# Kernel optimization log

Measured on AMD Instinct MI355X. Metric: run time of the kernel, lower is better.

## Reference

```python
import jax, jax.numpy as jnp
import numpy as np

N = 50000      # nodes
E = 400000     # edges (before self-loops)
IN = 128       # in_channels
OUT = 64       # out_channels (per-head; concat=False averages heads)
HEADS = 8      # heads of first GAT layer; second layer has 1 head
NEG_SLOPE = 0.2


def _glorot(key, shape, fan_in, fan_out):
    s = jnp.sqrt(2.0 / (fan_in + fan_out)).astype(jnp.float32)
    return jax.random.normal(key, shape, jnp.float32) * s


def setup_inputs() -> dict:
    key = jax.random.key(0)
    ks = jax.random.split(key, 10)
    x = jax.random.normal(ks[0], (N, IN), jnp.float32)
    edge_index = jax.random.randint(ks[1], (2, E), 0, N)
    # layer 1: heads=HEADS, per-head dim OUT
    W1 = _glorot(ks[2], (IN, HEADS * OUT), IN, HEADS * OUT)
    att_src1 = _glorot(ks[3], (HEADS, OUT), OUT, 1)
    att_dst1 = _glorot(ks[4], (HEADS, OUT), OUT, 1)
    b1 = jnp.zeros((OUT,), jnp.float32)
    # layer 2: heads=1
    W2 = _glorot(ks[5], (OUT, 1 * OUT), OUT, OUT)
    att_src2 = _glorot(ks[6], (1, OUT), OUT, 1)
    att_dst2 = _glorot(ks[7], (1, OUT), OUT, 1)
    b2 = jnp.zeros((OUT,), jnp.float32)
    return dict(x=x, edge_index=edge_index, W1=W1, att_src1=att_src1,
                att_dst1=att_dst1, b1=b1, W2=W2, att_src2=att_src2,
                att_dst2=att_dst2, b2=b2)


def gat_conv(x, edge_index, W, att_src, att_dst, bias, heads, ch):
    """PyG GATConv with concat=False (mean over heads), add_self_loops=True."""
    n = x.shape[0]
    loop = jnp.arange(n, dtype=edge_index.dtype)
    src = jnp.concatenate([edge_index[0], loop])  # [E+N]
    dst = jnp.concatenate([edge_index[1], loop])
    h = (x @ W).reshape(n, heads, ch)                     # [N, H, C]
    a_s = jnp.sum(h * att_src, axis=-1)                   # [N, H]
    a_d = jnp.sum(h * att_dst, axis=-1)                   # [N, H]
    e = jax.nn.leaky_relu(a_s[src] + a_d[dst], NEG_SLOPE)  # [E+N, H]
    # numerically stable segment softmax over incoming edges of each dst node
    emax = jax.lax.stop_gradient(
        jax.ops.segment_max(e, dst, num_segments=n))       # [N, H]
    ee = jnp.exp(e - emax[dst])
    denom = jax.ops.segment_sum(ee, dst, num_segments=n)  # [N, H]
    alpha = ee / denom[dst]                                # [E+N, H]
    out = jax.ops.segment_sum(alpha[:, :, None] * h[src], dst,
                              num_segments=n)              # [N, H, C]
    return out.mean(axis=1) + bias                         # [N, C]


def reference(x, edge_index, W1, att_src1, att_dst1, b1,
              W2, att_src2, att_dst2, b2):
    h = gat_conv(x, edge_index, W1, att_src1, att_dst1, b1, HEADS, OUT)
    h = jax.nn.elu(h)
    return gat_conv(h, edge_index, W2, att_src2, att_dst2, b2, 1, OUT)
```

## Files before the change

kernel.cpp:

```cpp
#include <hip/hip_runtime.h>
#include <cstdint>
#include <cstddef>

#define NEG_SLOPE 0.2f

typedef short bf16x8 __attribute__((ext_vector_type(8)));
typedef float f32x4 __attribute__((ext_vector_type(4)));
typedef float f32x2 __attribute__((ext_vector_type(2)));

__device__ __forceinline__ unsigned short f2bf(float f) {
  unsigned u = __float_as_uint(f);
  u = u + 0x7FFFu + ((u >> 16) & 1u);
  return (unsigned short)(u >> 16);
}
__device__ __forceinline__ float bf2f(unsigned short b) {
  return __uint_as_float((unsigned)b << 16);
}
__device__ __forceinline__ f32x2 unpk(unsigned xv) {
  f32x2 r;
  r.x = __uint_as_float(xv << 16);
  r.y = __uint_as_float(xv & 0xFFFF0000u);
  return r;
}
__device__ __forceinline__ float rlf(float v, int l) {
  return __uint_as_float(
      (unsigned)__builtin_amdgcn_readlane((int)__float_as_uint(v), l));
}
__device__ __forceinline__ void dma16(const unsigned short* g, unsigned short* l) {
  __builtin_amdgcn_global_load_lds(
      (const __attribute__((address_space(1))) unsigned*)g,
      (__attribute__((address_space(3))) unsigned*)l, 16, 0, 0);
}

__global__ __launch_bounds__(256) void prep_all(
    const int* __restrict__ ei, int* __restrict__ counts,
    const float* __restrict__ x, unsigned short* __restrict__ xb,
    const float* __restrict__ W1, const float* __restrict__ att_s1,
    const float* __restrict__ att_d1, unsigned short* __restrict__ AsAdT,
    unsigned short* __restrict__ WbT,
    const float* __restrict__ W2, unsigned short* __restrict__ W2t,
    const float* __restrict__ att_s2, const float* __restrict__ att_d2,
    float* __restrict__ AsAd2,
    int E, int ET, int N, int B0, int B1) {
  int b = blockIdx.x, tid = threadIdx.x;
  if (b < B0) {
    int i = b * 256 + tid;
    if (i < ET) {
      int dst = (i < E) ? ei[E + i] : (i - E);
      atomicAdd(&counts[dst], 1);
    }
    return;
  }
  b -= B0;
  if (b < B1) {
    int i = b * 256 + tid;
    if (i < N * 32) {
      float4 v = ((const float4*)x)[i];
      ushort4 o;
      o.x = f2bf(v.x); o.y = f2bf(v.y); o.z = f2bf(v.z); o.w = f2bf(v.w);
      ((ushort4*)xb)[i] = o;
    }
    return;
  }
  b -= B1;
  if (b < 8) {
    int i = b * 256 + tid;
    int o = i >> 7, k = i & 127, h = o & 7;
    const float* att = (o < 8) ? att_s1 : att_d1;
    float s = 0.f;
    for (int c = 0; c < 64; c++) s += W1[(size_t)k * 512 + h * 64 + c] * att[h * 64 + c];
    AsAdT[i] = f2bf(s);
    return;
  }
  b -= 8;
  if (b < 256) {
    int i = b * 256 + tid;
    int o = i >> 10, k = i & 1023, h = k >> 7, c = k & 127;
    WbT[i] = f2bf(W1[(size_t)c * 512 + h * 64 + o]);
    return;
  }
  b -= 256;
  if (b < 16) {
    int i = b * 256 + tid;
    if (i < 64 * 64) {
      int k = i >> 6, nn = i & 63;
      W2t[(size_t)nn * 64 + k] = f2bf(W2[i]);
    }
    return;
  }
  {
    int i = tid;
    if (i < 128) {
      int o = i >> 6, k = i & 63;
      const float* att = (o == 0) ? att_s2 : att_d2;
      float s = 0.f;
      for (int c = 0; c < 64; c++) s += W2[(size_t)k * 64 + c] * att[c];
      AsAd2[i] = s;
    }
  }
}

__global__ __launch_bounds__(1024) void scan_dots(
    const int* __restrict__ counts, int* __restrict__ offsets,
    const unsigned short* __restrict__ xb, const unsigned short* __restrict__ AsAdT,
    float* __restrict__ asd, int n) {
  if (blockIdx.x == 0) {
    __shared__ int sums[1024];
    int t = threadIdx.x;
    int chunk = (n + 1023) >> 10;
    int start = t * chunk;
    int end = min(start + chunk, n);
    int s = 0;
    for (int i = start; i < end; i++) s += counts[i];
    sums[t] = s;
    __syncthreads();
    for (int off = 1; off < 1024; off <<= 1) {
      int v = (t >= off) ? sums[t - off] : 0;
      __syncthreads();
      sums[t] += v;
      __syncthreads();
    }
    int run = sums[t] - s;
    for (int i = start; i < end; i++) { offsets[i] = run; run += counts[i]; }
    if (t == 1023) offsets[n] = sums[1023];
    return;
  }
  int tid = threadIdx.x;
  int wave = tid >> 6, lane = tid & 63;
  int q = lane >> 4, t = lane & 15;
  int row0 = (blockIdx.x - 1) * 256 + wave * 16;
  int arow = row0 + t; if (arow > n - 1) arow = n - 1;
  const bf16x8* aptr = (const bf16x8*)(xb + (size_t)arow * 128);
  const bf16x8* bptr = (const bf16x8*)(AsAdT + t * 128);
  f32x4 acc = (f32x4){0.f, 0.f, 0.f, 0.f};
  #pragma unroll
  for (int s = 0; s < 4; s++)
    acc = __builtin_amdgcn_mfma_f32_16x16x32_bf16(aptr[s * 4 + q], bptr[s * 4 + q],
                                                  acc, 0, 0, 0);
  #pragma unroll
  for (int r = 0; r < 4; r++) {
    int row = row0 + q * 4 + r;
    if (row < n) asd[row * 16 + t] = acc[r];
  }
}

__global__ __launch_bounds__(256) void fill_csr(
    const int* __restrict__ ei, const int* __restrict__ offsets,
    int* __restrict__ cursor, int* __restrict__ srcs, int E, int ET) {
  int i = blockIdx.x * 256 + threadIdx.x;
  if (i >= ET) return;
  int src, dst;
  if (i < E) { src = ei[i]; dst = ei[E + i]; } else { src = dst = i - E; }
  int pos = atomicAdd(&cursor[dst], 1);
  srcs[offsets[dst] + pos] = src;
}

#define CONSUME8(STG, W, ACC)                                         \
  _Pragma("unroll")                                                   \
  for (int k = 0; k < 8; k++) {                                       \
    unsigned xv = *(const unsigned*)&(STG)[k * 128 + 2 * lane];       \
    f32x2 x2 = unpk(xv);                                              \
    ACC[0] += x2 * rlf(W, k * 8 + 0);                                 \
    ACC[1] += x2 * rlf(W, k * 8 + 1);                                 \
    ACC[2] += x2 * rlf(W, k * 8 + 2);                                 \
    ACC[3] += x2 * rlf(W, k * 8 + 3);                                 \
    ACC[4] += x2 * rlf(W, k * 8 + 4);                                 \
    ACC[5] += x2 * rlf(W, k * 8 + 5);                                 \
    ACC[6] += x2 * rlf(W, k * 8 + 6);                                 \
    ACC[7] += x2 * rlf(W, k * 8 + 7);                                 \
  }

__global__ __launch_bounds__(512, 4) void agg1_gemm(
    const int* __restrict__ offsets, const int* __restrict__ srcs,
    const float* __restrict__ asd, const unsigned short* __restrict__ xb,
    const unsigned short* __restrict__ WbT, const float* __restrict__ b1,
    const float* __restrict__ AsAd2, unsigned short* __restrict__ zb,
    float* __restrict__ as2, float* __restrict__ ad2, int N) {
  __shared__ unsigned short sh[16 * 2048];
  int tid = threadIdx.x;
  int wv = tid >> 6, lane = tid & 63;
  int nb = blockIdx.x;
  {
    int nodeA = nb * 16 + 2 * wv;
    unsigned short* stgA = &sh[(2 * wv) * 2048];
    unsigned short* stgB = &sh[(2 * wv + 1) * 2048];
    f32x2 accA[8], accB[8];
    #pragma unroll
    for (int h = 0; h < 8; h++) {
      accA[h] = (f32x2){0.f, 0.f};
      accB[h] = (f32x2){0.f, 0.f};
    }
    float wslA = 0.f, wslB = 0.f;
    int begA = offsets[nodeA];
    int endA = offsets[nodeA + 1];
    int endB = offsets[nodeA + 2];
    int begB = endA;
    int jlA = endA - 1, jlB = endB - 1;
    float advA = asd[(size_t)nodeA * 16 + 8 + (lane & 7)];
    float advB = asd[(size_t)(nodeA + 1) * 16 + 8 + (lane & 7)];
    for (int c = 0;; c += 16) {
      int cbA = begA + c, cbB = begB + c;
      bool hA = cbA < endA, hB = cbB < endB;
      if (!hA && !hB) break;
      int cntA = endA - cbA, cntB = endB - cbB;
      int sA0 = 0, sA1 = 0, sA2 = 0, sA3 = 0;
      int sB0 = 0, sB1 = 0, sB2 = 0, sB3 = 0;
      float asvaA = 0.f, asvbA = 0.f, asvaB = 0.f, asvbB = 0.f;
      if (hA) {
        sA0 = srcs[min(cbA + (lane >> 4), jlA)];
        sA1 = srcs[min(cbA + 4 + (lane >> 4), jlA)];
        int sw = srcs[min(cbA + (lane >> 3), jlA)];
        asvaA = asd[(size_t)sw * 16 + (lane & 7)];
        if (cntA > 8) {
          sA2 = srcs[min(cbA + 8 + (lane >> 4), jlA)];
          sA3 = srcs[min(cbA + 12 + (lane >> 4), jlA)];
          int sw2 = srcs[min(cbA + 8 + (lane >> 3), jlA)];
          asvbA = asd[(size_t)sw2 * 16 + (lane & 7)];
        }
      }
      if (hB) {
        sB0 = srcs[min(cbB + (lane >> 4), jlB)];
        sB1 = srcs[min(cbB + 4 + (lane >> 4), jlB)];
        int sw = srcs[min(cbB + (lane >> 3), jlB)];
        asvaB = asd[(size_t)sw * 16 + (lane & 7)];
        if (cntB > 8) {
          sB2 = srcs[min(cbB + 8 + (lane >> 4), jlB)];
          sB3 = srcs[min(cbB + 12 + (lane >> 4), jlB)];
          int sw2 = srcs[min(cbB + 8 + (lane >> 3), jlB)];
          asvbB = asd[(size_t)sw2 * 16 + (lane & 7)];
        }
      }
      if (hA) {
        dma16(xb + (size_t)(unsigned)sA0 * 128 + (lane & 15) * 8, stgA);
        dma16(xb + (size_t)(unsigned)sA1 * 128 + (lane & 15) * 8, stgA + 512);
        if (cntA > 8) {
          dma16(xb + (size_t)(unsigned)sA2 * 128 + (lane & 15) * 8, stgA + 1024);
          dma16(xb + (size_t)(unsigned)sA3 * 128 + (lane & 15) * 8, stgA + 1536);
        }
      }
      if (hB) {
        dma16(xb + (size_t)(unsigned)sB0 * 128 + (lane & 15) * 8, stgB);
        dma16(xb + (size_t)(unsigned)sB1 * 128 + (lane & 15) * 8, stgB + 512);
        if (cntB > 8) {
          dma16(xb + (size_t)(unsigned)sB2 * 128 + (lane & 15) * 8, stgB + 1024);
          dma16(xb + (size_t)(unsigned)sB3 * 128 + (lane & 15) * 8, stgB + 1536);
        }
      }
      float waA = 0.f, wbA = 0.f, waB = 0.f, wbB = 0.f;
      if (hA) {
        float v = asvaA + advA;
        v = (v > 0.f) ? v : NEG_SLOPE * v;
        waA = (cbA + (lane >> 3) < endA) ? __expf(v) : 0.f;
        if (cntA > 8) {
          v = asvbA + advA;
          v = (v > 0.f) ? v : NEG_SLOPE * v;
          wbA = (cbA + 8 + (lane >> 3) < endA) ? __expf(v) : 0.f;
        }
      }
      if (hB) {
        float v = asvaB + advB;
        v = (v > 0.f) ? v : NEG_SLOPE * v;
        waB = (cbB + (lane >> 3) < endB) ? __expf(v) : 0.f;
        if (cntB > 8) {
          v = asvbB + advB;
          v = (v > 0.f) ? v : NEG_SLOPE * v;
          wbB = (cbB + 8 + (lane >> 3) < endB) ? __expf(v) : 0.f;
        }
      }
      wslA += waA + wbA;
      wslB += waB + wbB;
      __builtin_amdgcn_s_waitcnt(0x0f70);
      if (hA) {
        CONSUME8(stgA, waA, accA);
        if (cntA > 8) { CONSUME8((stgA + 1024), wbA, accA); }
      }
      if (hB) {
        CONSUME8(stgB, waB, accB);
        if (cntB > 8) { CONSUME8((stgB + 1024), wbB, accB); }
      }
    }
    wslA += __shfl_xor(wslA, 8, 64);
    wslA += __shfl_xor(wslA, 16, 64);
    wslA += __shfl_xor(wslA, 32, 64);
    wslB += __shfl_xor(wslB, 8, 64);
    wslB += __shfl_xor(wslB, 16, 64);
    wslB += __shfl_xor(wslB, 32, 64);
    __syncthreads();
    #pragma unroll
    for (int h = 0; h < 8; h++) {
      float ivA = 0.125f / rlf(wslA, h);
      unsigned oA = (unsigned)f2bf(accA[h].x * ivA) |
                    ((unsigned)f2bf(accA[h].y * ivA) << 16);
      *(unsigned*)&sh[(2 * wv) * 1032 + h * 128 + 2 * lane] = oA;
      float ivB = 0.125f / rlf(wslB, h);
      unsigned oB = (unsigned)f2bf(accB[h].x * ivB) |
                    ((unsigned)f2bf(accB[h].y * ivB) << 16);
      *(unsigned*)&sh[(2 * wv + 1) * 1032 + h * 128 + 2 * lane] = oB;
    }
  }
  __syncthreads();
  if (wv < 4) {
    int q = lane >> 4, t = lane & 15;
    f32x4 acc4 = (f32x4){0.f, 0.f, 0.f, 0.f};
    const unsigned short* bbase = WbT + (size_t)(wv * 16 + t) * 1024;
    #pragma unroll 8
    for (int s = 0; s < 32; s++) {
      bf16x8 af = *(const bf16x8*)&sh[t * 1032 + s * 32 + q * 8];
      bf16x8 bf = *(const bf16x8*)&bbase[s * 32 + q * 8];
      acc4 = __builtin_amdgcn_mfma_f32_16x16x32_bf16(af, bf, acc4, 0, 0, 0);
    }
    int col = wv * 16 + t;
    float bias = b1[col];
    float vs = AsAd2[col], vd = AsAd2[64 + col];
    #pragma unroll
    for (int r = 0; r < 4; r++) {
      int row = q * 4 + r;
      int node = nb * 16 + row;
      float v = acc4[r] + bias;
      v = (v > 0.f) ? v : (__expf(v) - 1.f);
      zb[(size_t)node * 64 + col] = f2bf(v);
      float s = v * vs, d = v * vd;
      #pragma unroll
      for (int off = 1; off < 16; off <<= 1) {
        s += __shfl_xor(s, off, 64);
        d += __shfl_xor(d, off, 64);
      }
      if (t == 0) {
        atomicAdd(&as2[node], s);
        atomicAdd(&ad2[node], d);
      }
    }
  }
}

__global__ __launch_bounds__(512, 8) void agg2_gemm(
    const int* __restrict__ offsets, const int* __restrict__ srcs,
    const float* __restrict__ as2, const float* __restrict__ ad2,
    const unsigned short* __restrict__ zb, const unsigned short* __restrict__ W2t,
    const float* __restrict__ b2, float* __restrict__ out, int N) {
  __shared__ unsigned short stg[16 * 1024];
  __shared__ unsigned short sh[16 * 72];
  int tid = threadIdx.x;
  int wv = tid >> 6, lane = tid & 63;
  int nb = blockIdx.x;
  {
    int nodeA = nb * 16 + 2 * wv;
    unsigned short* stA = &stg[(2 * wv) * 1024];
    unsigned short* stB = &stg[(2 * wv + 1) * 1024];
    f32x2 accA = (f32x2){0.f, 0.f}, accB = (f32x2){0.f, 0.f};
    float wslA = 0.f, wslB = 0.f;
    int begA = offsets[nodeA];
    int endA = offsets[nodeA + 1];
    int endB = offsets[nodeA + 2];
    int begB = endA;
    int jlA = endA - 1, jlB = endB - 1;
    float advA = ad2[nodeA];
    float advB = ad2[nodeA + 1];
    for (int c = 0;; c += 16) {
      int cbA = begA + c, cbB = begB + c;
      bool hA = cbA < endA, hB = cbB < endB;
      if (!hA && !hB) break;
      int cntA = endA - cbA, cntB = endB - cbB;
      float wlA = 0.f, wlB = 0.f;
      int sR0A = 0, sR1A = 0, sR0B = 0, sR1B = 0;
      float asvA = 0.f, asvB = 0.f;
      if (hA) {
        int sAll = srcs[min(cbA + (lane & 15), jlA)];
        asvA = as2[sAll];
        sR0A = srcs[min(cbA + (lane >> 3), jlA)];
        if (cntA > 8) sR1A = srcs[min(cbA + 8 + (lane >> 3), jlA)];
      }
      if (hB) {
        int sAll = srcs[min(cbB + (lane & 15), jlB)];
        asvB = as2[sAll];
        sR0B = srcs[min(cbB + (lane >> 3), jlB)];
        if (cntB > 8) sR1B = srcs[min(cbB + 8 + (lane >> 3), jlB)];
      }
      if (hA) {
        dma16(zb + (size_t)(unsigned)sR0A * 64 + (lane & 7) * 8, stA);
        if (cntA > 8)
          dma16(zb + (size_t)(unsigned)sR1A * 64 + (lane & 7) * 8, stA + 512);
      }
      if (hB) {
        dma16(zb + (size_t)(unsigned)sR0B * 64 + (lane & 7) * 8, stB);
        if (cntB > 8)
          dma16(zb + (size_t)(unsigned)sR1B * 64 + (lane & 7) * 8, stB + 512);
      }
      if (hA) {
        float v = asvA + advA;
        v = (v > 0.f) ? v : NEG_SLOPE * v;
        wlA = (cbA + (lane & 15) < endA) ? __expf(v) : 0.f;
      }
      if (hB) {
        float v = asvB + advB;
        v = (v > 0.f) ? v : NEG_SLOPE * v;
        wlB = (cbB + (lane & 15) < endB) ? __expf(v) : 0.f;
      }
      if (lane < 16) { wslA += wlA; wslB += wlB; }
      __builtin_amdgcn_s_waitcnt(0x0f70);
      if (hA) {
        #pragma unroll
        for (int k = 0; k < 4; k++) {
          float w0 = rlf(wlA, 2 * k);
          float w1 = rlf(wlA, 2 * k + 1);
          float w = (lane >= 32) ? w1 : w0;
          unsigned zv = *(const unsigned*)&stA[k * 128 + 2 * lane];
          accA += unpk(zv) * w;
        }
        if (cntA > 8) {
          #pragma unroll
          for (int k = 4; k < 8; k++) {
            float w0 = rlf(wlA, 2 * k);
            float w1 = rlf(wlA, 2 * k + 1);
            float w = (lane >= 32) ? w1 : w0;
            unsigned zv = *(const unsigned*)&stA[k * 128 + 2 * lane];
            accA += unpk(zv) * w;
          }
        }
      }
      if (hB) {
        #pragma unroll
        for (int k = 0; k < 4; k++) {
          float w0 = rlf(wlB, 2 * k);
          float w1 = rlf(wlB, 2 * k + 1);
          float w = (lane >= 32) ? w1 : w0;
          unsigned zv = *(const unsigned*)&stB[k * 128 + 2 * lane];
          accB += unpk(zv) * w;
        }
        if (cntB > 8) {
          #pragma unroll
          for (int k = 4; k < 8; k++) {
            float w0 = rlf(wlB, 2 * k);
            float w1 = rlf(wlB, 2 * k + 1);
            float w = (lane >= 32) ? w1 : w0;
            unsigned zv = *(const unsigned*)&stB[k * 128 + 2 * lane];
            accB += unpk(zv) * w;
          }
        }
      }
    }
    wslA += __shfl_xor(wslA, 1, 64);
    wslA += __shfl_xor(wslA, 2, 64);
    wslA += __shfl_xor(wslA, 4, 64);
    wslA += __shfl_xor(wslA, 8, 64);
    wslB += __shfl_xor(wslB, 1, 64);
    wslB += __shfl_xor(wslB, 2, 64);
    wslB += __shfl_xor(wslB, 4, 64);
    wslB += __shfl_xor(wslB, 8, 64);
    float totA = rlf(wslA, 0);
    float totB = rlf(wslB, 0);
    accA.x += __shfl_xor(accA.x, 32, 64);
    accA.y += __shfl_xor(accA.y, 32, 64);
    accB.x += __shfl_xor(accB.x, 32, 64);
    accB.y += __shfl_xor(accB.y, 32, 64);
    if (lane < 32) {
      float invA = 1.f / totA;
      unsigned oA = (unsigned)f2bf(accA.x * invA) |
                    ((unsigned)f2bf(accA.y * invA) << 16);
      *(unsigned*)&sh[(2 * wv) * 72 + 2 * lane] = oA;
      float invB = 1.f / totB;
      unsigned oB = (unsigned)f2bf(accB.x * invB) |
                    ((unsigned)f2bf(accB.y * invB) << 16);
      *(unsigned*)&sh[(2 * wv + 1) * 72 + 2 * lane] = oB;
    }
  }
  __syncthreads();
  if (wv < 4) {
    int q = lane >> 4, t = lane & 15;
    f32x4 acc4 = (f32x4){0.f, 0.f, 0.f, 0.f};
    const unsigned short* bbase = W2t + (size_t)(wv * 16 + t) * 64;
    #pragma unroll
    for (int s = 0; s < 2; s++) {
      bf16x8 af = *(const bf16x8*)&sh[t * 72 + s * 32 + q * 8];
      bf16x8 bf = *(const bf16x8*)&bbase[s * 32 + q * 8];
      acc4 = __builtin_amdgcn_mfma_f32_16x16x32_bf16(af, bf, acc4, 0, 0, 0);
    }
    int col = wv * 16 + t;
    float bias = b2[col];
    #pragma unroll
    for (int r = 0; r < 4; r++) {
      int node = nb * 16 + q * 4 + r;
      if (node < N) out[(size_t)node * 64 + col] = acc4[r] + bias;
    }
  }
}

extern "C" void kernel_launch(void* const* d_in, const int* in_sizes, int n_in,
                              void* d_out, int out_size, void* d_ws, size_t ws_size,
                              hipStream_t stream) {
  const int IN = 128;
  const int N = in_sizes[0] / IN;
  const int E = in_sizes[1] / 2;
  const int ET = E + N;

  const float* x        = (const float*)d_in[0];
  const int*   ei       = (const int*)d_in[1];
  const float* W1       = (const float*)d_in[2];
  const float* att_src1 = (const float*)d_in[3];
  const float* att_dst1 = (const float*)d_in[4];
  const float* b1       = (const float*)d_in[5];
  const float* W2       = (const float*)d_in[6];
  const float* att_src2 = (const float*)d_in[7];
  const float* att_dst2 = (const float*)d_in[8];
  const float* b2       = (const float*)d_in[9];
  float* out = (float*)d_out;

  char* base = (char*)d_ws;
  size_t off = 0;
  auto alloc = [&](size_t bytes) -> char* {
    char* p = base + off;
    off = (off + bytes + 255) & ~(size_t)255;
    return p;
  };
  unsigned short* xb    = (unsigned short*)alloc((size_t)N * 128 * 2);
  unsigned short* AsAdT = (unsigned short*)alloc((size_t)16 * 128 * 2);
  unsigned short* WbT   = (unsigned short*)alloc((size_t)64 * 1024 * 2);
  unsigned short* W2t   = (unsigned short*)alloc((size_t)64 * 64 * 2);
  unsigned short* zb    = (unsigned short*)alloc((size_t)N * 64 * 2);
  float* AsAd2 = (float*)alloc((size_t)128 * 4);
  float* asd1  = (float*)alloc((size_t)N * 16 * 4);
  int* offsets = (int*)alloc((size_t)(N + 1) * 4);
  int* srcs    = (int*)alloc((size_t)ET * 4);
  char* zero_begin = base + off;
  int* counts  = (int*)alloc((size_t)N * 4);
  int* cursor  = (int*)alloc((size_t)N * 4);
  float* a_s2  = (float*)alloc((size_t)N * 4);
  float* a_d2  = (float*)alloc((size_t)N * 4);
  char* zero_end = base + off;

  hipMemsetAsync(zero_begin, 0, (size_t)(zero_end - zero_begin), stream);

  const int TB = 256;
  auto cdiv = [](int a, int b) { return (a + b - 1) / b; };

  int B0 = cdiv(ET, TB);
  int B1 = cdiv(N * 32, TB);
  prep_all<<<B0 + B1 + 8 + 256 + 16 + 1, TB, 0, stream>>>(
      ei, counts, x, xb, W1, att_src1, att_dst1, AsAdT, WbT, W2, W2t,
      att_src2, att_dst2, AsAd2, E, ET, N, B0, B1);

  scan_dots<<<1 + cdiv(N, 256), 1024, 0, stream>>>(counts, offsets, xb, AsAdT,
                                                   asd1, N);

  fill_csr<<<cdiv(ET, TB), TB, 0, stream>>>(ei, offsets, cursor, srcs, E, ET);

  agg1_gemm<<<cdiv(N, 16), 512, 0, stream>>>(offsets, srcs, asd1, xb, WbT, b1,
                                             AsAd2, zb, a_s2, a_d2, N);

  agg2_gemm<<<cdiv(N, 16), 512, 0, stream>>>(offsets, srcs, a_s2, a_d2, zb,
                                             W2t, b2, out, N);
}
```

Before: 327.2 us.

## Gather neighbor rows into registers instead of LDS DMA; reuse histogram positions for CSR fill

```diff
diff --git a/kernel.cpp b/kernel.cpp
--- a/kernel.cpp
+++ b/kernel.cpp
@@ -26,14 +26,10 @@
   return __uint_as_float(
       (unsigned)__builtin_amdgcn_readlane((int)__float_as_uint(v), l));
 }
-__device__ __forceinline__ void dma16(const unsigned short* g, unsigned short* l) {
-  __builtin_amdgcn_global_load_lds(
-      (const __attribute__((address_space(1))) unsigned*)g,
-      (__attribute__((address_space(3))) unsigned*)l, 16, 0, 0);
-}
 
 __global__ __launch_bounds__(256) void prep_all(
     const int* __restrict__ ei, int* __restrict__ counts,
+    int* __restrict__ posb,
     const float* __restrict__ x, unsigned short* __restrict__ xb,
     const float* __restrict__ W1, const float* __restrict__ att_s1,
     const float* __restrict__ att_d1, unsigned short* __restrict__ AsAdT,
@@ -47,7 +43,8 @@
     int i = b * 256 + tid;
     if (i < ET) {
       int dst = (i < E) ? ei[E + i] : (i - E);
-      atomicAdd(&counts[dst], 1);
+      int pos = atomicAdd(&counts[dst], 1);
+      posb[i] = pos;
     }
     return;
   }
@@ -146,20 +143,18 @@
 
 __global__ __launch_bounds__(256) void fill_csr(
     const int* __restrict__ ei, const int* __restrict__ offsets,
-    int* __restrict__ cursor, int* __restrict__ srcs, int E, int ET) {
+    const int* __restrict__ posb, int* __restrict__ srcs, int E, int ET) {
   int i = blockIdx.x * 256 + threadIdx.x;
   if (i >= ET) return;
   int src, dst;
   if (i < E) { src = ei[i]; dst = ei[E + i]; } else { src = dst = i - E; }
-  int pos = atomicAdd(&cursor[dst], 1);
-  srcs[offsets[dst] + pos] = src;
-}
-
-#define CONSUME8(STG, W, ACC)                                         \
+  srcs[offsets[dst] + posb[i]] = src;
+}
+
+#define CONSUME8R(RV, W, ACC)                                         \
   _Pragma("unroll")                                                   \
   for (int k = 0; k < 8; k++) {                                       \
-    unsigned xv = *(const unsigned*)&(STG)[k * 128 + 2 * lane];       \
-    f32x2 x2 = unpk(xv);                                              \
+    f32x2 x2 = unpk(RV[k]);                                           \
     ACC[0] += x2 * rlf(W, k * 8 + 0);                                 \
     ACC[1] += x2 * rlf(W, k * 8 + 1);                                 \
     ACC[2] += x2 * rlf(W, k * 8 + 2);                                 \
@@ -176,14 +171,12 @@
     const unsigned short* __restrict__ WbT, const float* __restrict__ b1,
     const float* __restrict__ AsAd2, unsigned short* __restrict__ zb,
     float* __restrict__ as2, float* __restrict__ ad2, int N) {
-  __shared__ unsigned short sh[16 * 2048];
+  __shared__ unsigned short sh[16 * 1032];
   int tid = threadIdx.x;
   int wv = tid >> 6, lane = tid & 63;
   int nb = blockIdx.x;
   {
     int nodeA = nb * 16 + 2 * wv;
-    unsigned short* stgA = &sh[(2 * wv) * 2048];
-    unsigned short* stgB = &sh[(2 * wv + 1) * 2048];
     f32x2 accA[8], accB[8];
     #pragma unroll
     for (int h = 0; h < 8; h++) {
@@ -203,47 +196,53 @@
       bool hA = cbA < endA, hB = cbB < endB;
       if (!hA && !hB) break;
       int cntA = endA - cbA, cntB = endB - cbB;
-      int sA0 = 0, sA1 = 0, sA2 = 0, sA3 = 0;
-      int sB0 = 0, sB1 = 0, sB2 = 0, sB3 = 0;
+      int sAllA = 0, sAllB = 0;
       float asvaA = 0.f, asvbA = 0.f, asvaB = 0.f, asvbB = 0.f;
       if (hA) {
-        sA0 = srcs[min(cbA + (lane >> 4), jlA)];
-        sA1 = srcs[min(cbA + 4 + (lane >> 4), jlA)];
-        int sw = srcs[min(cbA + (lane >> 3), jlA)];
-        asvaA = asd[(size_t)sw * 16 + (lane & 7)];
+        sAllA = srcs[min(cbA + (lane & 15), jlA)];
+        int swa = srcs[min(cbA + (lane >> 3), jlA)];
+        asvaA = asd[(size_t)(unsigned)swa * 16 + (lane & 7)];
         if (cntA > 8) {
-          sA2 = srcs[min(cbA + 8 + (lane >> 4), jlA)];
-          sA3 = srcs[min(cbA + 12 + (lane >> 4), jlA)];
-          int sw2 = srcs[min(cbA + 8 + (lane >> 3), jlA)];
-          asvbA = asd[(size_t)sw2 * 16 + (lane & 7)];
-        }
-      }
-      if (hB) {
-        sB0 = srcs[min(cbB + (lane >> 4), jlB)];
-        sB1 = srcs[min(cbB + 4 + (lane >> 4), jlB)];
-        int sw = srcs[min(cbB + (lane >> 3), jlB)];
-        asvaB = asd[(size_t)sw * 16 + (lane & 7)];
+          int swb = srcs[min(cbA + 8 + (lane >> 3), jlA)];
+          asvbA = asd[(size_t)(unsigned)swb * 16 + (lane & 7)];
+        }
+      }
+      if (hB) {
+        sAllB = srcs[min(cbB + (lane & 15), jlB)];
+        int swa = srcs[min(cbB + (lane >> 3), jlB)];
+        asvaB = asd[(size_t)(unsigned)swa * 16 + (lane & 7)];
         if (cntB > 8) {
-          sB2 = srcs[min(cbB + 8 + (lane >> 4), jlB)];
-          sB3 = srcs[min(cbB + 12 + (lane >> 4), jlB)];
-          int sw2 = srcs[min(cbB + 8 + (lane >> 3), jlB)];
-          asvbB = asd[(size_t)sw2 * 16 + (lane & 7)];
-        }
-      }
-      if (hA) {
-        dma16(xb + (size_t)(unsigned)sA0 * 128 + (lane & 15) * 8, stgA);
-        dma16(xb + (size_t)(unsigned)sA1 * 128 + (lane & 15) * 8, stgA + 512);
+          int swb = srcs[min(cbB + 8 + (lane >> 3), jlB)];
+          asvbB = asd[(size_t)(unsigned)swb * 16 + (lane & 7)];
+        }
+      }
+      unsigned rvaA[8], rvbA[8], rvaB[8], rvbB[8];
+      if (hA) {
+        #pragma unroll
+        for (int k = 0; k < 8; k++) {
+          int se = __builtin_amdgcn_readlane(sAllA, k);
+          rvaA[k] = *(const unsigned*)&xb[(size_t)(unsigned)se * 128 + 2 * lane];
+        }
         if (cntA > 8) {
-          dma16(xb + (size_t)(unsigned)sA2 * 128 + (lane & 15) * 8, stgA + 1024);
-          dma16(xb + (size_t)(unsigned)sA3 * 128 + (lane & 15) * 8, stgA + 1536);
-        }
-      }
-      if (hB) {
-        dma16(xb + (size_t)(unsigned)sB0 * 128 + (lane & 15) * 8, stgB);
-        dma16(xb + (size_t)(unsigned)sB1 * 128 + (lane & 15) * 8, stgB + 512);
+          #pragma unroll
+          for (int k = 0; k < 8; k++) {
+            int se = __builtin_amdgcn_readlane(sAllA, k + 8);
+            rvbA[k] = *(const unsigned*)&xb[(size_t)(unsigned)se * 128 + 2 * lane];
+          }
+        }
+      }
+      if (hB) {
+        #pragma unroll
+        for (int k = 0; k < 8; k++) {
+          int se = __builtin_amdgcn_readlane(sAllB, k);
+          rvaB[k] = *(const unsigned*)&xb[(size_t)(unsigned)se * 128 + 2 * lane];
+        }
         if (cntB > 8) {
-          dma16(xb + (size_t)(unsigned)sB2 * 128 + (lane & 15) * 8, stgB + 1024);
-          dma16(xb + (size_t)(unsigned)sB3 * 128 + (lane & 15) * 8, stgB + 1536);
+          #pragma unroll
+          for (int k = 0; k < 8; k++) {
+            int se = __builtin_amdgcn_readlane(sAllB, k + 8);
+            rvbB[k] = *(const unsigned*)&xb[(size_t)(unsigned)se * 128 + 2 * lane];
+          }
         }
       }
       float waA = 0.f, wbA = 0.f, waB = 0.f, wbB = 0.f;
@@ -269,14 +268,13 @@
       }
       wslA += waA + wbA;
       wslB += waB + wbB;
-      __builtin_amdgcn_s_waitcnt(0x0f70);
-      if (hA) {
-        CONSUME8(stgA, waA, accA);
-        if (cntA > 8) { CONSUME8((stgA + 1024), wbA, accA); }
-      }
-      if (hB) {
-        CONSUME8(stgB, waB, accB);
-        if (cntB > 8) { CONSUME8((stgB + 1024), wbB, accB); }
+      if (hA) {
+        CONSUME8R(rvaA, waA, accA);
+        if (cntA > 8) { CONSUME8R(rvbA, wbA, accA); }
+      }
+      if (hB) {
+        CONSUME8R(rvaB, waB, accB);
+        if (cntB > 8) { CONSUME8R(rvbB, wbB, accB); }
       }
     }
     wslA += __shfl_xor(wslA, 8, 64);
@@ -285,7 +283,6 @@
     wslB += __shfl_xor(wslB, 8, 64);
     wslB += __shfl_xor(wslB, 16, 64);
     wslB += __shfl_xor(wslB, 32, 64);
-    __syncthreads();
     #pragma unroll
     for (int h = 0; h < 8; h++) {
       float ivA = 0.125f / rlf(wslA, h);
@@ -333,59 +330,80 @@
   }
 }
 
-__global__ __launch_bounds__(512, 8) void agg2_gemm(
+__global__ __launch_bounds__(512, 4) void agg2_gemm(
     const int* __restrict__ offsets, const int* __restrict__ srcs,
     const float* __restrict__ as2, const float* __restrict__ ad2,
     const unsigned short* __restrict__ zb, const unsigned short* __restrict__ W2t,
     const float* __restrict__ b2, float* __restrict__ out, int N) {
-  __shared__ unsigned short stg[16 * 1024];
   __shared__ unsigned short sh[16 * 72];
   int tid = threadIdx.x;
   int wv = tid >> 6, lane = tid & 63;
   int nb = blockIdx.x;
   {
     int nodeA = nb * 16 + 2 * wv;
-    unsigned short* stA = &stg[(2 * wv) * 1024];
-    unsigned short* stB = &stg[(2 * wv + 1) * 1024];
-    f32x2 accA = (f32x2){0.f, 0.f}, accB = (f32x2){0.f, 0.f};
-    float wslA = 0.f, wslB = 0.f;
+    int half = lane >> 5;
+    float advA = ad2[nodeA];
+    float advB = ad2[nodeA + 1];
     int begA = offsets[nodeA];
     int endA = offsets[nodeA + 1];
     int endB = offsets[nodeA + 2];
     int begB = endA;
     int jlA = endA - 1, jlB = endB - 1;
-    float advA = ad2[nodeA];
-    float advB = ad2[nodeA + 1];
+    f32x2 accA = (f32x2){0.f, 0.f}, accB = (f32x2){0.f, 0.f};
+    float wslA = 0.f, wslB = 0.f;
     for (int c = 0;; c += 16) {
       int cbA = begA + c, cbB = begB + c;
       bool hA = cbA < endA, hB = cbB < endB;
       if (!hA && !hB) break;
       int cntA = endA - cbA, cntB = endB - cbB;
+      int sAllA = 0, sAllB = 0;
+      float asvA = 0.f, asvB = 0.f;
+      if (hA) {
+        sAllA = srcs[min(cbA + (lane & 15), jlA)];
+        asvA = as2[sAllA];
+      }
+      if (hB) {
+        sAllB = srcs[min(cbB + (lane & 15), jlB)];
+        asvB = as2[sAllB];
+      }
+      unsigned rvA[8], rvB[8];
+      if (hA) {
+        #pragma unroll
+        for (int k = 0; k < 4; k++) {
+          int s0 = __builtin_amdgcn_readlane(sAllA, 2 * k);
+          int s1 = __builtin_amdgcn_readlane(sAllA, 2 * k + 1);
+          int se = half ? s1 : s0;
+          rvA[k] = *(const unsigned*)&zb[(size_t)(unsigned)se * 64 + 2 * (lane & 31)];
+        }
+        if (cntA > 8) {
+          #pragma unroll
+          for (int k = 4; k < 8; k++) {
+            int s0 = __builtin_amdgcn_readlane(sAllA, 2 * k);
+            int s1 = __builtin_amdgcn_readlane(sAllA, 2 * k + 1);
+            int se = half ? s1 : s0;
+            rvA[k] = *(const unsigned*)&zb[(size_t)(unsigned)se * 64 + 2 * (lane & 31)];
+          }
+        }
+      }
+      if (hB) {
+        #pragma unroll
+        for (int k = 0; k < 4; k++) {
+          int s0 = __builtin_amdgcn_readlane(sAllB, 2 * k);
+          int s1 = __builtin_amdgcn_readlane(sAllB, 2 * k + 1);
+          int se = half ? s1 : s0;
+          rvB[k] = *(const unsigned*)&zb[(size_t)(unsigned)se * 64 + 2 * (lane & 31)];
+        }
+        if (cntB > 8) {
+          #pragma unroll
+          for (int k = 4; k < 8; k++) {
+            int s0 = __builtin_amdgcn_readlane(sAllB, 2 * k);
+            int s1 = __builtin_amdgcn_readlane(sAllB, 2 * k + 1);
+            int se = half ? s1 : s0;
+            rvB[k] = *(const unsigned*)&zb[(size_t)(unsigned)se * 64 + 2 * (lane & 31)];
+          }
+        }
+      }
       float wlA = 0.f, wlB = 0.f;
-      int sR0A = 0, sR1A = 0, sR0B = 0, sR1B = 0;
-      float asvA = 0.f, asvB = 0.f;
-      if (hA) {
-        int sAll = srcs[min(cbA + (lane & 15), jlA)];
-        asvA = as2[sAll];
-        sR0A = srcs[min(cbA + (lane >> 3), jlA)];
-        if (cntA > 8) sR1A = srcs[min(cbA + 8 + (lane >> 3), jlA)];
-      }
-      if (hB) {
-        int sAll = srcs[min(cbB + (lane & 15), jlB)];
-        asvB = as2[sAll];
-        sR0B = srcs[min(cbB + (lane >> 3), jlB)];
-        if (cntB > 8) sR1B = srcs[min(cbB + 8 + (lane >> 3), jlB)];
-      }
-      if (hA) {
-        dma16(zb + (size_t)(unsigned)sR0A * 64 + (lane & 7) * 8, stA);
-        if (cntA > 8)
-          dma16(zb + (size_t)(unsigned)sR1A * 64 + (lane & 7) * 8, stA + 512);
-      }
-      if (hB) {
-        dma16(zb + (size_t)(unsigned)sR0B * 64 + (lane & 7) * 8, stB);
-        if (cntB > 8)
-          dma16(zb + (size_t)(unsigned)sR1B * 64 + (lane & 7) * 8, stB + 512);
-      }
       if (hA) {
         float v = asvA + advA;
         v = (v > 0.f) ? v : NEG_SLOPE * v;
@@ -397,24 +415,21 @@
         wlB = (cbB + (lane & 15) < endB) ? __expf(v) : 0.f;
       }
       if (lane < 16) { wslA += wlA; wslB += wlB; }
-      __builtin_amdgcn_s_waitcnt(0x0f70);
       if (hA) {
         #pragma unroll
         for (int k = 0; k < 4; k++) {
           float w0 = rlf(wlA, 2 * k);
           float w1 = rlf(wlA, 2 * k + 1);
-          float w = (lane >= 32) ? w1 : w0;
-          unsigned zv = *(const unsigned*)&stA[k * 128 + 2 * lane];
-          accA += unpk(zv) * w;
+          float w = half ? w1 : w0;
+          accA += unpk(rvA[k]) * w;
         }
         if (cntA > 8) {
           #pragma unroll
           for (int k = 4; k < 8; k++) {
             float w0 = rlf(wlA, 2 * k);
             float w1 = rlf(wlA, 2 * k + 1);
-            float w = (lane >= 32) ? w1 : w0;
-            unsigned zv = *(const unsigned*)&stA[k * 128 + 2 * lane];
-            accA += unpk(zv) * w;
+            float w = half ? w1 : w0;
+            accA += unpk(rvA[k]) * w;
           }
         }
       }
@@ -423,18 +438,16 @@
         for (int k = 0; k < 4; k++) {
           float w0 = rlf(wlB, 2 * k);
           float w1 = rlf(wlB, 2 * k + 1);
-          float w = (lane >= 32) ? w1 : w0;
-          unsigned zv = *(const unsigned*)&stB[k * 128 + 2 * lane];
-          accB += unpk(zv) * w;
+          float w = half ? w1 : w0;
+          accB += unpk(rvB[k]) * w;
         }
         if (cntB > 8) {
           #pragma unroll
           for (int k = 4; k < 8; k++) {
             float w0 = rlf(wlB, 2 * k);
             float w1 = rlf(wlB, 2 * k + 1);
-            float w = (lane >= 32) ? w1 : w0;
-            unsigned zv = *(const unsigned*)&stB[k * 128 + 2 * lane];
-            accB += unpk(zv) * w;
+            float w = half ? w1 : w0;
+            accB += unpk(rvB[k]) * w;
           }
         }
       }
@@ -521,9 +534,9 @@
   float* asd1  = (float*)alloc((size_t)N * 16 * 4);
   int* offsets = (int*)alloc((size_t)(N + 1) * 4);
   int* srcs    = (int*)alloc((size_t)ET * 4);
+  int* posb    = (int*)alloc((size_t)ET * 4);
   char* zero_begin = base + off;
   int* counts  = (int*)alloc((size_t)N * 4);
-  int* cursor  = (int*)alloc((size_t)N * 4);
   float* a_s2  = (float*)alloc((size_t)N * 4);
   float* a_d2  = (float*)alloc((size_t)N * 4);
   char* zero_end = base + off;
@@ -536,13 +549,13 @@
   int B0 = cdiv(ET, TB);
   int B1 = cdiv(N * 32, TB);
   prep_all<<<B0 + B1 + 8 + 256 + 16 + 1, TB, 0, stream>>>(
-      ei, counts, x, xb, W1, att_src1, att_dst1, AsAdT, WbT, W2, W2t,
+      ei, counts, posb, x, xb, W1, att_src1, att_dst1, AsAdT, WbT, W2, W2t,
       att_src2, att_dst2, AsAd2, E, ET, N, B0, B1);
 
   scan_dots<<<1 + cdiv(N, 256), 1024, 0, stream>>>(counts, offsets, xb, AsAdT,
                                                    asd1, N);
 
-  fill_csr<<<cdiv(ET, TB), TB, 0, stream>>>(ei, offsets, cursor, srcs, E, ET);
+  fill_csr<<<cdiv(ET, TB), TB, 0, stream>>>(ei, offsets, posb, srcs, E, ET);
 
   agg1_gemm<<<cdiv(N, 16), 512, 0, stream>>>(offsets, srcs, asd1, xb, WbT, b1,
                                              AsAd2, zb, a_s2, a_d2, N);
```

Measured after the change: 310.8 us. -5.0%, faster.
